# Performance work log

Hardware: AMD Instinct MI355X
Metric: run time of the kernel (lower is better)

Reference implementation:

```python
import jax, jax.numpy as jnp
import numpy as np

N, L, E, H = 8, 2048, 1024, 1024
EPS = 1e-5


def layernorm(x, g, b):
    m = jnp.mean(x, axis=-1, keepdims=True)
    v = jnp.var(x, axis=-1, keepdims=True)
    return (x - m) * jax.lax.rsqrt(v + EPS) * g + b


def setup_inputs() -> dict:
    key = jax.random.key(0)
    ks = jax.random.split(key, 6)
    s = 0.02
    return {
        "X": jax.random.normal(ks[0], (N, L, E), dtype=jnp.float32),
        "Wq": jax.random.normal(ks[1], (E, H), dtype=jnp.float32) * s,
        "bq": jnp.zeros((H,), jnp.float32),
        "Wk": jax.random.normal(ks[2], (E, H), dtype=jnp.float32) * s,
        "bk": jnp.zeros((H,), jnp.float32),
        "Wv": jax.random.normal(ks[3], (E, H), dtype=jnp.float32) * s,
        "bv": jnp.zeros((H,), jnp.float32),
        "Wf": jax.random.normal(ks[4], (H, H), dtype=jnp.float32) * s,
        "bf": jnp.zeros((H,), jnp.float32),
        "g1": jnp.ones((H,), jnp.float32),
        "b1": jnp.zeros((H,), jnp.float32),
        "g2": jnp.ones((H,), jnp.float32),
        "b2": jnp.zeros((H,), jnp.float32),
    }


def reference(X, Wq, bq, Wk, bk, Wv, bv, Wf, bf, g1, b1, g2, b2):
    scale = 1.0 / jnp.sqrt(jnp.float32(H))
    # both Q and K scaled by 1/sqrt(H) as in source (effective 1/H)
    Q = (X @ Wq + bq) * scale          # (N, L, H)
    K = (X @ Wk + bk) * scale          # (N, L, H)
    V = X @ Wv + bv                    # (N, L, H)
    A = jnp.einsum('nah,nbh->nab', Q, K)   # (N, Lq, Lk)
    A = jax.nn.softmax(A, axis=1)           # softmax over QUERY axis (dim=1), as in source
    # einsum('nll,nlh->nlh') = diagonal of A scaling V elementwise
    diag = jnp.diagonal(A, axis1=1, axis2=2)  # (N, L)
    O = diag[..., None] * V                   # (N, L, H)
    h = layernorm(O + X, g1, b1)
    h = layernorm(h @ Wf + bf + h, g2, b2)
    return h
```

## Files before the change

### kernel.cpp

```cpp
#include <hip/hip_runtime.h>
#include <math.h>

#define NB   8
#define LLEN 2048
#define HDIM 1024
#define LNEPS 1e-5f

#define BM 256
#define BN 256
#define BK 64
#define NT_K (HDIM / BK)
#define NT_K8 (HDIM / 128)
#define NTHR 512
#define SLOT (BM * BK)
#define SLOT8 32768

typedef __attribute__((ext_vector_type(8))) short short8;
typedef __attribute__((ext_vector_type(4))) unsigned short ushort4v;
typedef __attribute__((ext_vector_type(4))) float f32x4;
typedef __attribute__((ext_vector_type(4))) int int4v;
typedef __attribute__((ext_vector_type(8))) int int8v;
typedef __attribute__((ext_vector_type(8))) unsigned char uchar8;

typedef __attribute__((address_space(3))) void lds_void;
typedef const __attribute__((address_space(1))) void glob_void;

__device__ __forceinline__ unsigned short f2bf(float f) {
    union { float f; unsigned u; } v; v.f = f;
    unsigned r = v.u + 0x7FFFu + ((v.u >> 16) & 1u);
    return (unsigned short)(r >> 16);
}
__device__ __forceinline__ float bf2f(unsigned short h) {
    union { unsigned u; float f; } v; v.u = ((unsigned)h) << 16;
    return v.f;
}

__device__ __forceinline__ unsigned char f2fp8(float x) {
    union { float f; unsigned u; } v; v.f = x;
    unsigned s = (v.u >> 24) & 0x80u;
    float a = fabsf(x);
    if (!(a < 448.f)) return (unsigned char)(s | 0x7E);
    int e = (int)((v.u >> 23) & 0xFF) - 127;
    if (e < -6) e = -6;
    float q = rintf(ldexpf(a, 3 - e));
    if (q >= 16.f) { q *= 0.5f; e += 1; }
    int qi = (int)q;
    unsigned byte = (qi < 8) ? (unsigned)qi
                             : (((unsigned)(e + 7) << 3) | (unsigned)(qi - 8));
    return (unsigned char)(s | byte);
}
__device__ __forceinline__ float fp8d(unsigned char b) {
    int e = (b >> 3) & 15, m = b & 7;
    float v = e ? ldexpf((float)(8 + m), e - 10) : ldexpf((float)m, -9);
    return (b & 0x80) ? -v : v;
}

__device__ __forceinline__ unsigned pack4_fp8(float a, float b, float c, float d) {
#if __has_builtin(__builtin_amdgcn_cvt_pk_fp8_f32)
    int r = __builtin_amdgcn_cvt_pk_fp8_f32(a, b, 0, false);
    r = __builtin_amdgcn_cvt_pk_fp8_f32(c, d, r, true);
    return (unsigned)r;
#else
    return (unsigned)f2fp8(a) | ((unsigned)f2fp8(b) << 8)
         | ((unsigned)f2fp8(c) << 16) | ((unsigned)f2fp8(d) << 24);
#endif
}

__device__ __forceinline__ void wg_barrier() {
    asm volatile("" ::: "memory");
    __builtin_amdgcn_s_barrier();
    asm volatile("" ::: "memory");
}

__device__ __forceinline__ void stage_tile(
    const unsigned short* __restrict__ src, int R0, int kcol0,
    unsigned short* ldsDst, int w, int lane)
{
    const int rsub = lane >> 3;
    const int csw  = 8 * ((lane & 7) ^ rsub);
    #pragma unroll
    for (int s = 0; s < 4; ++s) {
        const int r = (s*8 + w)*8 + rsub;
        const unsigned short* g = src + (size_t)(R0 + r) * HDIM + kcol0 + csw;
        __builtin_amdgcn_global_load_lds(
            (glob_void*)g, (lds_void*)(ldsDst + (s*8 + w)*512), 16, 0, 0);
    }
}

__device__ __forceinline__ void run_pipeline(
    const unsigned short* __restrict__ srcA,
    const unsigned short* __restrict__ srcB,
    int rowBase, int colBase,
    unsigned short* lds, f32x4 (&acc)[8][4])
{
    const int t = threadIdx.x, w = t >> 6, l = t & 63;
    const int wr = w >> 2, wc = w & 3;
    const int lr = l & 15;
    const int sw = (l & 7) << 4;
    const int aRB = (wr*128 + lr) * 128;
    const int bRB = (wc*64  + lr) * 128;
    const int c0 = ((l >> 4) * 16) ^ sw;
    const int c1 = (64 + ((l >> 4) * 16)) ^ sw;

    unsigned short* sA[2] = { lds,            lds + 2*SLOT };
    unsigned short* sB[2] = { lds + SLOT,     lds + 3*SLOT };

    stage_tile(srcA, rowBase, 0,  sA[0], w, l);
    stage_tile(srcB, colBase, 0,  sB[0], w, l);
    stage_tile(srcA, rowBase, BK, sA[1], w, l);
    stage_tile(srcB, colBase, BK, sB[1], w, l);
    asm volatile("s_waitcnt vmcnt(8)" ::: "memory");
    wg_barrier();

    for (int kt = 0; kt < NT_K; ++kt) {
        const char* bufA = (const char*)sA[kt & 1];
        const char* bufB = (const char*)sB[kt & 1];
        #pragma unroll
        for (int kk = 0; kk < 2; ++kk) {
            const int cc = kk ? c1 : c0;
            short8 af[8], bfr[4];
            #pragma unroll
            for (int mi = 0; mi < 8; ++mi)
                af[mi] = *(const short8*)(bufA + aRB + mi*2048 + cc);
            #pragma unroll
            for (int ni = 0; ni < 4; ++ni)
                bfr[ni] = *(const short8*)(bufB + bRB + ni*2048 + cc);
            #pragma unroll
            for (int mi = 0; mi < 8; ++mi)
                #pragma unroll
                for (int ni = 0; ni < 4; ++ni)
                    acc[mi][ni] = __builtin_amdgcn_mfma_f32_16x16x32_bf16(
                        af[mi], bfr[ni], acc[mi][ni], 0, 0, 0);
        }
        if (kt == NT_K - 1) break;
        wg_barrier();
        if (kt + 2 < NT_K) {
            stage_tile(srcA, rowBase, (kt+2)*BK, sA[kt&1], w, l);
            stage_tile(srcB, colBase, (kt+2)*BK, sB[kt&1], w, l);
            asm volatile("s_waitcnt vmcnt(8)" ::: "memory");
        } else {
            asm volatile("s_waitcnt vmcnt(0)" ::: "memory");
        }
        wg_barrier();
    }
}

__device__ __forceinline__ void stage_tile8(
    const unsigned char* __restrict__ src, int R0, int kcol0,
    unsigned char* ldsDst, int w, int lane)
{
    const int rsub = lane >> 3;
    const int csw  = ((lane & 7) ^ rsub) << 4;
    #pragma unroll
    for (int s = 0; s < 4; ++s) {
        const int r = (s*8 + w)*8 + rsub;
        __builtin_amdgcn_global_load_lds(
            (glob_void*)(src + (size_t)(R0 + r) * HDIM + kcol0 + csw),
            (lds_void*)(ldsDst + (s*8 + w)*1024), 16, 0, 0);
    }
}

__device__ __forceinline__ void run_pipeline_fp8(
    const unsigned char* __restrict__ srcA,
    const unsigned char* __restrict__ srcB,
    int rowBase, int colBase,
    unsigned char* lds, f32x4 (&acc)[8][4],
    unsigned sa, unsigned sb)
{
    const int t = threadIdx.x, w = t >> 6, l = t & 63;
    const int wr = w >> 2, wc = w & 3;
    const int lr = l & 15;
    const int sw = (l & 7) << 4;
    const int aRB = (wr*128 + lr) * 128;
    const int bRB = (wc*64  + lr) * 128;
    const int g0 = (l >> 4) * 32;
    const int cc0 = g0 ^ sw;
    const int cc1 = (g0 + 16) ^ sw;

    unsigned char* sA[2] = { lds,             lds + 2*SLOT8 };
    unsigned char* sB[2] = { lds + SLOT8,     lds + 3*SLOT8 };

    stage_tile8(srcA, rowBase, 0,   sA[0], w, l);
    stage_tile8(srcB, colBase, 0,   sB[0], w, l);
    stage_tile8(srcA, rowBase, 128, sA[1], w, l);
    stage_tile8(srcB, colBase, 128, sB[1], w, l);
    asm volatile("s_waitcnt vmcnt(8)" ::: "memory");
    wg_barrier();

    for (int kt = 0; kt < NT_K8; ++kt) {
        const char* bufA = (const char*)sA[kt & 1];
        const char* bufB = (const char*)sB[kt & 1];
        int8v b8[4];
        #pragma unroll
        for (int ni = 0; ni < 4; ++ni)
            b8[ni] = __builtin_shufflevector(
                *(const int4v*)(bufB + bRB + ni*2048 + cc0),
                *(const int4v*)(bufB + bRB + ni*2048 + cc1),
                0, 1, 2, 3, 4, 5, 6, 7);
        #pragma unroll
        for (int mi = 0; mi < 8; ++mi) {
            int8v a8 = __builtin_shufflevector(
                *(const int4v*)(bufA + aRB + mi*2048 + cc0),
                *(const int4v*)(bufA + aRB + mi*2048 + cc1),
                0, 1, 2, 3, 4, 5, 6, 7);
            #pragma unroll
            for (int ni = 0; ni < 4; ++ni)
                acc[mi][ni] = __builtin_amdgcn_mfma_scale_f32_16x16x128_f8f6f4(
                    a8, b8[ni], acc[mi][ni], 0, 0, 0, sa, 0, sb);
        }
        if (kt == NT_K8 - 1) break;
        wg_barrier();
        if (kt + 2 < NT_K8) {
            stage_tile8(srcA, rowBase, (kt+2)*128, sA[kt&1], w, l);
            stage_tile8(srcB, colBase, (kt+2)*128, sB[kt&1], w, l);
            asm volatile("s_waitcnt vmcnt(8)" ::: "memory");
        } else {
            asm volatile("s_waitcnt vmcnt(0)" ::: "memory");
        }
        wg_barrier();
    }
}

__global__ __launch_bounds__(NTHR, 2) void gemm_proj(
    const unsigned short* __restrict__ A,
    const unsigned short* __restrict__ Bt,
    const float* __restrict__ bias0, const float* __restrict__ bias1,
    const float* __restrict__ bias2,
    unsigned short* __restrict__ C0, unsigned short* __restrict__ C1,
    unsigned short* __restrict__ C2,
    unsigned char* __restrict__ C8,
    float al0, float al1, float al2, int gx)
{
    __shared__ __align__(16) unsigned short lds[4 * SLOT];
    const int nwg = gridDim.x, bid = blockIdx.x;
    const int swz = (bid & 7) * (nwg >> 3) + (bid >> 3);
    const int bx = swz % gx, by = swz / gx;
    const int rowBase = by * BM, colBase = bx * BN;

    f32x4 acc[8][4] = {};
    run_pipeline(A, Bt, rowBase, colBase, lds, acc);

    const int t = threadIdx.x, w = t >> 6, l = t & 63;
    const int wr = w >> 2, wc = w & 3;
    const int lr = l & 15;

    const int mat = colBase >> 10;
    unsigned short* Cm = (mat == 0) ? C0 : (mat == 1 ? C1 : C2);
    const float* bm    = (mat == 0) ? bias0 : (mat == 1 ? bias1 : bias2);
    const float am     = (mat == 0) ? al0 : (mat == 1 ? al1 : al2);
    const int lcb = colBase & (HDIM - 1);

    if (mat == 0 && C8) {
        #pragma unroll
        for (int ni = 0; ni < 4; ++ni) {
            const int col = lcb + wc*64 + ni*16 + lr;
            const float bv = bm[col];
            #pragma unroll
            for (int mi = 0; mi < 8; ++mi) {
                const int row0 = rowBase + wr*128 + mi*16 + (l >> 4) * 4;
                const unsigned wd = pack4_fp8(
                    am * (acc[mi][ni][0] + bv), am * (acc[mi][ni][1] + bv),
                    am * (acc[mi][ni][2] + bv), am * (acc[mi][ni][3] + bv));
                #pragma unroll
                for (int j = 0; j < 4; ++j)
                    C8[(size_t)(row0 + j) * HDIM + col] = (unsigned char)(wd >> (8*j));
            }
        }
        return;
    }

    #pragma unroll
    for (int ni = 0; ni < 4; ++ni) {
        const int col = lcb + wc*64 + ni*16 + lr;
        const float bv = bm[col];
        #pragma unroll
        for (int mi = 0; mi < 8; ++mi) {
            const int row0 = rowBase + wr*128 + mi*16 + (l >> 4) * 4;
            #pragma unroll
            for (int j = 0; j < 4; ++j)
                Cm[(size_t)(row0 + j) * HDIM + col] = f2bf(am * (acc[mi][ni][j] + bv));
        }
    }
}

__global__ __launch_bounds__(NTHR, 2) void gemm_proj_fp8(
    const unsigned char* __restrict__ A,
    const unsigned char* __restrict__ Bt,
    const float* __restrict__ bias0, const float* __restrict__ bias1,
    unsigned char* __restrict__ C0, unsigned char* __restrict__ C1,
    float al0, float al1, unsigned sb0, unsigned sb1, int gx)
{
    __shared__ __align__(16) unsigned char lds8[4 * SLOT8];
    const int nwg = gridDim.x, bid = blockIdx.x;
    const int swz = (bid & 7) * (nwg >> 3) + (bid >> 3);
    const int bx = swz % gx, by = swz / gx;
    const int rowBase = by * BM, colBase = bx * BN;

    const int mat = colBase >> 10;

    f32x4 acc[8][4] = {};
    run_pipeline_fp8(A, Bt, rowBase, colBase, lds8, acc,
                     0x7F7F7F7Fu, mat ? sb1 : sb0);

    const int t = threadIdx.x, w = t >> 6, l = t & 63;
    const int wr = w >> 2, wc = w & 3;
    const int lr = l & 15;

    unsigned char* Cm  = mat ? C1 : C0;
    const float* bm    = mat ? bias1 : bias0;
    const float am     = mat ? al1 : al0;
    const int lcb = colBase & (HDIM - 1);

    #pragma unroll
    for (int ni = 0; ni < 4; ++ni) {
        const int col = lcb + wc*64 + ni*16 + lr;
        const float bv = bm[col];
        #pragma unroll
        for (int mi = 0; mi < 8; ++mi) {
            const int row0 = rowBase + wr*128 + mi*16 + (l >> 4) * 4;
            const unsigned wd = pack4_fp8(
                am * (acc[mi][ni][0] + bv), am * (acc[mi][ni][1] + bv),
                am * (acc[mi][ni][2] + bv), am * (acc[mi][ni][3] + bv));
            #pragma unroll
            for (int j = 0; j < 4; ++j)
                Cm[(size_t)(row0 + j) * HDIM + col] = (unsigned char)(wd >> (8*j));
        }
    }
}

__global__ __launch_bounds__(NTHR, 2) void qk_colsum_diag_fp8(
    const unsigned char* __restrict__ Xq8,
    const unsigned char* __restrict__ Xb8,
    const float* __restrict__ uvec,
    float* __restrict__ colsum, float* __restrict__ diagv)
{
    __shared__ __align__(16) unsigned char lds8[4 * SLOT8];
    const int bid = blockIdx.x;
    const int n = bid & 7;
    const int rem = bid >> 3;
    const int rowBase = (rem & 7) * BM;
    const int colBase = (rem >> 3) * BN;
    const unsigned char* An = Xq8 + (size_t)n * LLEN * HDIM;
    const unsigned char* Bn = Xb8 + (size_t)n * LLEN * HDIM;

    f32x4 acc[8][4] = {};
    run_pipeline_fp8(An, Bn, rowBase, colBase, lds8, acc,
                     0x75757575u, 0x7F7F7F7Fu);

    const int t = threadIdx.x, w = t >> 6, l = t & 63;
    const int wr = w >> 2, wc = w & 3;
    const int lr = l & 15;

    float ur[8][4];
    #pragma unroll
    for (int mi = 0; mi < 8; ++mi)
        #pragma unroll
        for (int j = 0; j < 4; ++j)
            ur[mi][j] = uvec[(size_t)n * LLEN + rowBase + wr*128 + mi*16 + (l>>4)*4 + j];

    #pragma unroll
    for (int ni = 0; ni < 4; ++ni) {
        float s = 0.f;
        #pragma unroll
        for (int mi = 0; mi < 8; ++mi)
            #pragma unroll
            for (int j = 0; j < 4; ++j)
                s += __expf(acc[mi][ni][j] + ur[mi][j]);
        s += __shfl_xor(s, 16);
        s += __shfl_xor(s, 32);
        if (l < 16)
            atomicAdd(&colsum[(size_t)n * LLEN + colBase + wc*64 + ni*16 + l], s);
    }

    if (rowBase == colBase && (wc >> 1) == wr) {
        #pragma unroll
        for (int mi = 0; mi < 8; ++mi)
            #pragma unroll
            for (int ni = 0; ni < 4; ++ni)
                #pragma unroll
                for (int j = 0; j < 4; ++j) {
                    const int rr = wr*128 + mi*16 + (l >> 4)*4 + j;
                    const int cc = wc*64 + ni*16 + lr;
                    if (rr == cc)
                        diagv[(size_t)n * LLEN + rowBase + rr] = acc[mi][ni][j];
                }
    }
}

__global__ __launch_bounds__(256) void cast_x_dual(
    const float* __restrict__ in, unsigned short* __restrict__ outb,
    unsigned char* __restrict__ out8, int n8)
{
    int i = blockIdx.x * 256 + threadIdx.x;
    if (i >= n8) return;
    const float4* p = reinterpret_cast<const float4*>(in) + (size_t)i * 2;
    float4 a = p[0], b = p[1];
    short8 o;
    o[0] = (short)f2bf(a.x); o[1] = (short)f2bf(a.y);
    o[2] = (short)f2bf(a.z); o[3] = (short)f2bf(a.w);
    o[4] = (short)f2bf(b.x); o[5] = (short)f2bf(b.y);
    o[6] = (short)f2bf(b.z); o[7] = (short)f2bf(b.w);
    unsigned w0 = pack4_fp8(a.x, a.y, a.z, a.w);
    unsigned w1 = pack4_fp8(b.x, b.y, b.z, b.w);
    *(reinterpret_cast<short8*>(outb) + i) = o;
    uint2 pk; pk.x = w0; pk.y = w1;
    *(reinterpret_cast<uint2*>(out8) + i) = pk;
}

__global__ __launch_bounds__(256) void cast_f32_bf16(
    const float* __restrict__ in, unsigned short* __restrict__ outp, int n8)
{
    int i = blockIdx.x * 256 + threadIdx.x;
    if (i >= n8) return;
    const float4* p = reinterpret_cast<const float4*>(in) + (size_t)i * 2;
    float4 a = p[0], b = p[1];
    short8 o;
    o[0] = (short)f2bf(a.x); o[1] = (short)f2bf(a.y);
    o[2] = (short)f2bf(a.z); o[3] = (short)f2bf(a.w);
    o[4] = (short)f2bf(b.x); o[5] = (short)f2bf(b.y);
    o[6] = (short)f2bf(b.z); o[7] = (short)f2bf(b.w);
    *(reinterpret_cast<short8*>(outp) + i) = o;
}

__global__ __launch_bounds__(256) void transpose_cast_bf16(
    const float* __restrict__ W, unsigned short* __restrict__ Wt)
{
    __shared__ float tile[32][33];
    const int tx = threadIdx.x & 31, ty = threadIdx.x >> 5;
    const int c0 = blockIdx.x * 32, r0 = blockIdx.y * 32;
    #pragma unroll
    for (int r = 0; r < 4; ++r)
        tile[ty + r*8][tx] = W[(size_t)(r0 + ty + r*8) * HDIM + c0 + tx];
    __syncthreads();
    #pragma unroll
    for (int r = 0; r < 4; ++r)
        Wt[(size_t)(c0 + ty + r*8) * HDIM + r0 + tx] = f2bf(tile[tx][ty + r*8]);
}

__global__ __launch_bounds__(256) void transpose_cast_fp8(
    const float* __restrict__ W, unsigned char* __restrict__ Wt, float scale)
{
    __shared__ float tile[32][33];
    const int tx = threadIdx.x & 31, ty = threadIdx.x >> 5;
    const int c0 = blockIdx.x * 32, r0 = blockIdx.y * 32;
    #pragma unroll
    for (int r = 0; r < 4; ++r)
        tile[ty + r*8][tx] = W[(size_t)(r0 + ty + r*8) * HDIM + c0 + tx];
    __syncthreads();
    #pragma unroll
    for (int r = 0; r < 4; ++r)
        Wt[(size_t)(c0 + ty + r*8) * HDIM + r0 + tx] = f2fp8(tile[tx][ty + r*8] * scale);
}

__global__ __launch_bounds__(256) void pvec_kernel(
    const float* __restrict__ Wq, const float* __restrict__ bk,
    float* __restrict__ p)
{
    const int row = blockIdx.x * 4 + (threadIdx.x >> 6);
    const int l = threadIdx.x & 63;
    float s = 0.f;
    #pragma unroll
    for (int c = 0; c < HDIM; c += 64)
        s += Wq[(size_t)row * HDIM + c + l] * bk[c + l];
    #pragma unroll
    for (int off = 32; off > 0; off >>= 1) s += __shfl_down(s, off);
    if (l == 0) p[row] = s;
}

__global__ __launch_bounds__(256) void uvec_kernel(
    const unsigned short* __restrict__ Xb, const float* __restrict__ p,
    float* __restrict__ u, float sc2)
{
    const int row = blockIdx.x * 4 + (threadIdx.x >> 6);
    const int l = threadIdx.x & 63;
    const unsigned short* xr = Xb + (size_t)row * HDIM + l * 16;
    float s = 0.f;
    #pragma unroll
    for (int k = 0; k < 2; ++k) {
        short8 v = *reinterpret_cast<const short8*>(xr + k*8);
        #pragma unroll
        for (int j = 0; j < 8; ++j)
            s += bf2f((unsigned short)v[j]) * p[l*16 + k*8 + j];
    }
    #pragma unroll
    for (int off = 32; off > 0; off >>= 1) s += __shfl_down(s, off);
    if (l == 0) u[row] = s * sc2;
}

__global__ __launch_bounds__(256) void ln1_kernel(
    const unsigned char* __restrict__ V8, const unsigned short* __restrict__ Xbp,
    const float* __restrict__ colsum, const float* __restrict__ diagval,
    const float* __restrict__ uvec,
    const float* __restrict__ g1, const float* __restrict__ b1,
    unsigned short* __restrict__ h1)
{
    const int row = blockIdx.x;
    const size_t base = (size_t)row * HDIM;
    const float dv = __expf(diagval[row] + uvec[row]) / colsum[row];
    const int h0 = threadIdx.x * 4;

    unsigned vv = *reinterpret_cast<const unsigned*>(&V8[base + h0]);
    ushort4v xx = *reinterpret_cast<const ushort4v*>(&Xbp[base + h0]);
    float y[4];
    y[0] = dv * fp8d((unsigned char)(vv      )) + bf2f(xx[0]);
    y[1] = dv * fp8d((unsigned char)(vv >>  8)) + bf2f(xx[1]);
    y[2] = dv * fp8d((unsigned char)(vv >> 16)) + bf2f(xx[2]);
    y[3] = dv * fp8d((unsigned char)(vv >> 24)) + bf2f(xx[3]);

    float s = y[0]+y[1]+y[2]+y[3];
    float s2 = y[0]*y[0]+y[1]*y[1]+y[2]*y[2]+y[3]*y[3];
    #pragma unroll
    for (int off = 32; off > 0; off >>= 1) {
        s  += __shfl_down(s,  off);
        s2 += __shfl_down(s2, off);
    }
    __shared__ float ws1[4], ws2[4];
    const int wid = threadIdx.x >> 6;
    if ((threadIdx.x & 63) == 0) { ws1[wid] = s; ws2[wid] = s2; }
    __syncthreads();
    const float S  = ws1[0]+ws1[1]+ws1[2]+ws1[3];
    const float S2 = ws2[0]+ws2[1]+ws2[2]+ws2[3];
    const float m   = S  * (1.0f / HDIM);
    const float var = S2 * (1.0f / HDIM) - m*m;
    const float inv = rsqrtf(var + LNEPS);

    float4 gg = *reinterpret_cast<const float4*>(&g1[h0]);
    float4 bb = *reinterpret_cast<const float4*>(&b1[h0]);
    ushort4v o;
    o[0] = f2bf((y[0]-m)*inv*gg.x + bb.x);
    o[1] = f2bf((y[1]-m)*inv*gg.y + bb.y);
    o[2] = f2bf((y[2]-m)*inv*gg.z + bb.z);
    o[3] = f2bf((y[3]-m)*inv*gg.w + bb.w);
    *reinterpret_cast<ushort4v*>(&h1[base + h0]) = o;
}

__global__ __launch_bounds__(256) void ln2_kernel(
    const unsigned short* __restrict__ Gb, const unsigned short* __restrict__ h1b,
    const float* __restrict__ g2, const float* __restrict__ b2,
    float* __restrict__ out)
{
    const int row = blockIdx.x;
    const size_t base = (size_t)row * HDIM;
    const int h0 = threadIdx.x * 4;

    ushort4v gv = *reinterpret_cast<const ushort4v*>(&Gb[base + h0]);
    ushort4v hv = *reinterpret_cast<const ushort4v*>(&h1b[base + h0]);
    float y[4];
    y[0] = bf2f(gv[0]) + bf2f(hv[0]); y[1] = bf2f(gv[1]) + bf2f(hv[1]);
    y[2] = bf2f(gv[2]) + bf2f(hv[2]); y[3] = bf2f(gv[3]) + bf2f(hv[3]);

    float s = y[0]+y[1]+y[2]+y[3];
    float s2 = y[0]*y[0]+y[1]*y[1]+y[2]*y[2]+y[3]*y[3];
    #pragma unroll
    for (int off = 32; off > 0; off >>= 1) {
        s  += __shfl_down(s,  off);
        s2 += __shfl_down(s2, off);
    }
    __shared__ float ws1[4], ws2[4];
    const int wid = threadIdx.x >> 6;
    if ((threadIdx.x & 63) == 0) { ws1[wid] = s; ws2[wid] = s2; }
    __syncthreads();
    const float S  = ws1[0]+ws1[1]+ws1[2]+ws1[3];
    const float S2 = ws2[0]+ws2[1]+ws2[2]+ws2[3];
    const float m   = S  * (1.0f / HDIM);
    const float var = S2 * (1.0f / HDIM) - m*m;
    const float inv = rsqrtf(var + LNEPS);

    float4 gg = *reinterpret_cast<const float4*>(&g2[h0]);
    float4 bb = *reinterpret_cast<const float4*>(&b2[h0]);
    float4 o;
    o.x = (y[0]-m)*inv*gg.x + bb.x;
    o.y = (y[1]-m)*inv*gg.y + bb.y;
    o.z = (y[2]-m)*inv*gg.z + bb.z;
    o.w = (y[3]-m)*inv*gg.w + bb.w;
    *reinterpret_cast<float4*>(&out[base + h0]) = o;
}

extern "C" void kernel_launch(void* const* d_in, const int* in_sizes, int n_in,
                              void* d_out, int out_size, void* d_ws, size_t ws_size,
                              hipStream_t stream) {
    (void)in_sizes; (void)n_in; (void)out_size; (void)ws_size;
    const float* X  = (const float*)d_in[0];
    const float* Wq = (const float*)d_in[1];
    const float* bq = (const float*)d_in[2];   (void)bq;
    const float* Wk = (const float*)d_in[3];
    const float* bk = (const float*)d_in[4];
    const float* Wv = (const float*)d_in[5];
    const float* bv = (const float*)d_in[6];
    const float* Wf = (const float*)d_in[7];
    const float* bf = (const float*)d_in[8];
    const float* g1 = (const float*)d_in[9];
    const float* b1 = (const float*)d_in[10];
    const float* g2 = (const float*)d_in[11];
    const float* b2 = (const float*)d_in[12];
    float* out = (float*)d_out;

    const size_t MATE = (size_t)NB * LLEN * HDIM;
    const size_t WE   = (size_t)HDIM * HDIM;

    unsigned short* Xb  = (unsigned short*)d_out;
    unsigned char*  V8  = (unsigned char*)(Xb + MATE);

    unsigned short* h1b   = (unsigned short*)d_ws;
    unsigned short* Gb    = h1b + MATE;
    unsigned short* WfT   = Gb + MATE;
    unsigned short* Wqb   = WfT + WE;
    unsigned short* Wkb   = Wqb + WE;
    unsigned char*  Wqk8T = (unsigned char*)(Wkb + WE);
    unsigned char*  Wv8T  = Wqk8T + WE;
    float* colsum = (float*)(Wv8T + WE);
    float* diagv  = colsum + (size_t)NB * LLEN;
    float* pv     = diagv + (size_t)NB * LLEN;
    float* uv     = pv + HDIM;
    float* zvec   = uv + (size_t)NB * LLEN;
    unsigned char* Xq8 = (unsigned char*)(zvec + HDIM);
    unsigned char* Xb8 = Xq8 + MATE;

    const int M = NB * LLEN;
    const float sc2 = 1.0f / 1024.0f;

    hipMemsetAsync(colsum, 0, (size_t)NB * LLEN * sizeof(float), stream);
    hipMemsetAsync(zvec, 0, HDIM * sizeof(float), stream);

    cast_x_dual<<<(int)(MATE/8) / 256, 256, 0, stream>>>(X, Xb, Xb8, (int)(MATE/8));
    cast_f32_bf16<<<(int)(WE/8) / 256, 256, 0, stream>>>(Wq, Wqb, (int)(WE/8));
    cast_f32_bf16<<<(int)(WE/8) / 256, 256, 0, stream>>>(Wk, Wkb, (int)(WE/8));

    {
        dim3 tgrid(HDIM / 32, HDIM / 32);
        transpose_cast_bf16<<<tgrid, 256, 0, stream>>>(Wf, WfT);
        transpose_cast_fp8<<<tgrid, 256, 0, stream>>>(Wv, Wv8T, 16.0f);
    }

    gemm_proj<<<16, NTHR, 0, stream>>>(Wkb, Wqb, zvec, zvec, zvec,
                                       nullptr, nullptr, nullptr, Wqk8T,
                                       64.0f, 64.0f, 64.0f, 4);

    pvec_kernel<<<HDIM / 4, 256, 0, stream>>>(Wq, bk, pv);
    uvec_kernel<<<M / 4, 256, 0, stream>>>(Xb, pv, uv, sc2);

    {
        const int gx = 2 * HDIM / BN;
        const int nwg = gx * (M / BM);
        gemm_proj_fp8<<<nwg, NTHR, 0, stream>>>(Xb8, Wqk8T, zvec, bv,
                                                Xq8, V8, 1024.0f, 1.0f,
                                                0x6F6F6F6Fu ,
                                                0x7B7B7B7Bu , gx);
    }

    qk_colsum_diag_fp8<<<512, NTHR, 0, stream>>>(Xq8, Xb8, uv, colsum, diagv);

    ln1_kernel<<<M, 256, 0, stream>>>(V8, Xb, colsum, diagv, uv, g1, b1, h1b);

    {
        const int gx = HDIM / BN;
        const int nwg = gx * (M / BM);
        gemm_proj<<<nwg, NTHR, 0, stream>>>(h1b, WfT, bf, bf, bf,
                                            Gb, Gb, Gb, (unsigned char*)nullptr,
                                            1.0f, 1.0f, 1.0f, gx);
    }

    ln2_kernel<<<M, 256, 0, stream>>>(Gb, h1b, g2, b2, out);
}
```

Before: 247.8 us.

## Split-K the Wk·Wqᵀ weight product across more workgroups and merge small launches

The 1024x1024 Wk·Wqᵀ product ran on only 16 workgroups. It now splits K four ways across 64 workgroups that write fp32 partial slabs, followed by a reduce kernel that sums the slabs, scales and packs to fp8. The two weight casts are merged into one launch, and the two memsets into one larger memset. The aim is better CU utilisation on a small GEMM in exchange for extra fp32 slab traffic and one more launch. gemm_proj is simplified to a single output.

```diff
diff --git a/kernel.cpp b/kernel.cpp
--- a/kernel.cpp
+++ b/kernel.cpp
@@ -90,7 +90,7 @@
 __device__ __forceinline__ void run_pipeline(
     const unsigned short* __restrict__ srcA,
     const unsigned short* __restrict__ srcB,
-    int rowBase, int colBase,
+    int rowBase, int colBase, int k0, int nt,
     unsigned short* lds, f32x4 (&acc)[8][4])
 {
     const int t = threadIdx.x, w = t >> 6, l = t & 63;
@@ -105,14 +105,14 @@
     unsigned short* sA[2] = { lds,            lds + 2*SLOT };
     unsigned short* sB[2] = { lds + SLOT,     lds + 3*SLOT };
 
-    stage_tile(srcA, rowBase, 0,  sA[0], w, l);
-    stage_tile(srcB, colBase, 0,  sB[0], w, l);
-    stage_tile(srcA, rowBase, BK, sA[1], w, l);
-    stage_tile(srcB, colBase, BK, sB[1], w, l);
+    stage_tile(srcA, rowBase, k0,      sA[0], w, l);
+    stage_tile(srcB, colBase, k0,      sB[0], w, l);
+    stage_tile(srcA, rowBase, k0 + BK, sA[1], w, l);
+    stage_tile(srcB, colBase, k0 + BK, sB[1], w, l);
     asm volatile("s_waitcnt vmcnt(8)" ::: "memory");
     wg_barrier();
 
-    for (int kt = 0; kt < NT_K; ++kt) {
+    for (int kt = 0; kt < nt; ++kt) {
         const char* bufA = (const char*)sA[kt & 1];
         const char* bufB = (const char*)sB[kt & 1];
         #pragma unroll
@@ -132,11 +132,11 @@
                     acc[mi][ni] = __builtin_amdgcn_mfma_f32_16x16x32_bf16(
                         af[mi], bfr[ni], acc[mi][ni], 0, 0, 0);
         }
-        if (kt == NT_K - 1) break;
+        if (kt == nt - 1) break;
         wg_barrier();
-        if (kt + 2 < NT_K) {
-            stage_tile(srcA, rowBase, (kt+2)*BK, sA[kt&1], w, l);
-            stage_tile(srcB, colBase, (kt+2)*BK, sB[kt&1], w, l);
+        if (kt + 2 < nt) {
+            stage_tile(srcA, rowBase, k0 + (kt+2)*BK, sA[kt&1], w, l);
+            stage_tile(srcB, colBase, k0 + (kt+2)*BK, sB[kt&1], w, l);
             asm volatile("s_waitcnt vmcnt(8)" ::: "memory");
         } else {
             asm volatile("s_waitcnt vmcnt(0)" ::: "memory");
@@ -224,12 +224,9 @@
 __global__ __launch_bounds__(NTHR, 2) void gemm_proj(
     const unsigned short* __restrict__ A,
     const unsigned short* __restrict__ Bt,
-    const float* __restrict__ bias0, const float* __restrict__ bias1,
-    const float* __restrict__ bias2,
-    unsigned short* __restrict__ C0, unsigned short* __restrict__ C1,
-    unsigned short* __restrict__ C2,
-    unsigned char* __restrict__ C8,
-    float al0, float al1, float al2, int gx)
+    const float* __restrict__ bias,
+    unsigned short* __restrict__ C,
+    float alpha, int gx)
 {
     __shared__ __align__(16) unsigned short lds[4 * SLOT];
     const int nwg = gridDim.x, bid = blockIdx.x;
@@ -238,49 +235,69 @@
     const int rowBase = by * BM, colBase = bx * BN;
 
     f32x4 acc[8][4] = {};
-    run_pipeline(A, Bt, rowBase, colBase, lds, acc);
+    run_pipeline(A, Bt, rowBase, colBase, 0, NT_K, lds, acc);
 
     const int t = threadIdx.x, w = t >> 6, l = t & 63;
     const int wr = w >> 2, wc = w & 3;
     const int lr = l & 15;
 
-    const int mat = colBase >> 10;
-    unsigned short* Cm = (mat == 0) ? C0 : (mat == 1 ? C1 : C2);
-    const float* bm    = (mat == 0) ? bias0 : (mat == 1 ? bias1 : bias2);
-    const float am     = (mat == 0) ? al0 : (mat == 1 ? al1 : al2);
-    const int lcb = colBase & (HDIM - 1);
-
-    if (mat == 0 && C8) {
-        #pragma unroll
-        for (int ni = 0; ni < 4; ++ni) {
-            const int col = lcb + wc*64 + ni*16 + lr;
-            const float bv = bm[col];
-            #pragma unroll
-            for (int mi = 0; mi < 8; ++mi) {
-                const int row0 = rowBase + wr*128 + mi*16 + (l >> 4) * 4;
-                const unsigned wd = pack4_fp8(
-                    am * (acc[mi][ni][0] + bv), am * (acc[mi][ni][1] + bv),
-                    am * (acc[mi][ni][2] + bv), am * (acc[mi][ni][3] + bv));
-                #pragma unroll
-                for (int j = 0; j < 4; ++j)
-                    C8[(size_t)(row0 + j) * HDIM + col] = (unsigned char)(wd >> (8*j));
-            }
-        }
-        return;
-    }
-
     #pragma unroll
     for (int ni = 0; ni < 4; ++ni) {
-        const int col = lcb + wc*64 + ni*16 + lr;
-        const float bv = bm[col];
+        const int col = colBase + wc*64 + ni*16 + lr;
+        const float bv = bias[col];
         #pragma unroll
         for (int mi = 0; mi < 8; ++mi) {
             const int row0 = rowBase + wr*128 + mi*16 + (l >> 4) * 4;
             #pragma unroll
             for (int j = 0; j < 4; ++j)
-                Cm[(size_t)(row0 + j) * HDIM + col] = f2bf(am * (acc[mi][ni][j] + bv));
+                C[(size_t)(row0 + j) * HDIM + col] = f2bf(alpha * (acc[mi][ni][j] + bv));
         }
     }
+}
+
+__global__ __launch_bounds__(NTHR, 2) void gemm_wqk_splitk(
+    const unsigned short* __restrict__ Wkb,
+    const unsigned short* __restrict__ Wqb,
+    float* __restrict__ slabs)
+{
+    __shared__ __align__(16) unsigned short lds[4 * SLOT];
+    const int bid = blockIdx.x;
+    const int kz = bid & 3, tile = bid >> 2;
+    const int rowBase = (tile >> 2) * BM, colBase = (tile & 3) * BN;
+
+    f32x4 acc[8][4] = {};
+    run_pipeline(Wkb, Wqb, rowBase, colBase, kz * (HDIM/4), NT_K/4, lds, acc);
+
+    float* out = slabs + (size_t)kz * HDIM * HDIM;
+    const int t = threadIdx.x, w = t >> 6, l = t & 63;
+    const int wr = w >> 2, wc = w & 3;
+    const int lr = l & 15;
+
+    #pragma unroll
+    for (int ni = 0; ni < 4; ++ni) {
+        const int col = colBase + wc*64 + ni*16 + lr;
+        #pragma unroll
+        for (int mi = 0; mi < 8; ++mi) {
+            const int row0 = rowBase + wr*128 + mi*16 + (l >> 4) * 4;
+            #pragma unroll
+            for (int j = 0; j < 4; ++j)
+                out[(size_t)(row0 + j) * HDIM + col] = acc[mi][ni][j];
+        }
+    }
+}
+
+__global__ __launch_bounds__(256) void wqk_reduce_cast(
+    const float* __restrict__ slabs, unsigned char* __restrict__ out8)
+{
+    const size_t WEl = (size_t)HDIM * HDIM;
+    const size_t i = ((size_t)blockIdx.x * 256 + threadIdx.x) * 4;
+    float4 a = *reinterpret_cast<const float4*>(slabs + i);
+    float4 b = *reinterpret_cast<const float4*>(slabs + WEl + i);
+    float4 c = *reinterpret_cast<const float4*>(slabs + 2*WEl + i);
+    float4 d = *reinterpret_cast<const float4*>(slabs + 3*WEl + i);
+    unsigned wd = pack4_fp8(64.f*(a.x+b.x+c.x+d.x), 64.f*(a.y+b.y+c.y+d.y),
+                            64.f*(a.z+b.z+c.z+d.z), 64.f*(a.w+b.w+c.w+d.w));
+    *reinterpret_cast<unsigned*>(out8 + i) = wd;
 }
 
 __global__ __launch_bounds__(NTHR, 2) void gemm_proj_fp8(
@@ -407,11 +424,14 @@
     *(reinterpret_cast<uint2*>(out8) + i) = pk;
 }
 
-__global__ __launch_bounds__(256) void cast_f32_bf16(
-    const float* __restrict__ in, unsigned short* __restrict__ outp, int n8)
+__global__ __launch_bounds__(256) void cast_w2(
+    const float* __restrict__ W0, const float* __restrict__ W1,
+    unsigned short* __restrict__ out0, unsigned short* __restrict__ out1, int n8)
 {
     int i = blockIdx.x * 256 + threadIdx.x;
     if (i >= n8) return;
+    const float* in = blockIdx.y ? W1 : W0;
+    unsigned short* outp = blockIdx.y ? out1 : out0;
     const float4* p = reinterpret_cast<const float4*>(in) + (size_t)i * 2;
     float4 a = p[0], b = p[1];
     short8 o;
@@ -615,26 +635,27 @@
     float* zvec   = uv + (size_t)NB * LLEN;
     unsigned char* Xq8 = (unsigned char*)(zvec + HDIM);
     unsigned char* Xb8 = Xq8 + MATE;
+    float* wqkSlabs = (float*)(Xb8 + MATE);
 
     const int M = NB * LLEN;
     const float sc2 = 1.0f / 1024.0f;
 
-    hipMemsetAsync(colsum, 0, (size_t)NB * LLEN * sizeof(float), stream);
-    hipMemsetAsync(zvec, 0, HDIM * sizeof(float), stream);
+    const size_t mset = (3*(size_t)NB*LLEN + 2*HDIM) * sizeof(float);
+    hipMemsetAsync(colsum, 0, mset, stream);
 
     cast_x_dual<<<(int)(MATE/8) / 256, 256, 0, stream>>>(X, Xb, Xb8, (int)(MATE/8));
-    cast_f32_bf16<<<(int)(WE/8) / 256, 256, 0, stream>>>(Wq, Wqb, (int)(WE/8));
-    cast_f32_bf16<<<(int)(WE/8) / 256, 256, 0, stream>>>(Wk, Wkb, (int)(WE/8));
-
+    {
+        dim3 cg((int)(WE/8) / 256, 2);
+        cast_w2<<<cg, 256, 0, stream>>>(Wq, Wk, Wqb, Wkb, (int)(WE/8));
+    }
     {
         dim3 tgrid(HDIM / 32, HDIM / 32);
         transpose_cast_bf16<<<tgrid, 256, 0, stream>>>(Wf, WfT);
         transpose_cast_fp8<<<tgrid, 256, 0, stream>>>(Wv, Wv8T, 16.0f);
     }
 
-    gemm_proj<<<16, NTHR, 0, stream>>>(Wkb, Wqb, zvec, zvec, zvec,
-                                       nullptr, nullptr, nullptr, Wqk8T,
-                                       64.0f, 64.0f, 64.0f, 4);
+    gemm_wqk_splitk<<<64, NTHR, 0, stream>>>(Wkb, Wqb, wqkSlabs);
+    wqk_reduce_cast<<<(int)(WE/4) / 256, 256, 0, stream>>>(wqkSlabs, Wqk8T);
 
     pvec_kernel<<<HDIM / 4, 256, 0, stream>>>(Wq, bk, pv);
     uvec_kernel<<<M / 4, 256, 0, stream>>>(Xb, pv, uv, sc2);
@@ -655,9 +676,7 @@
     {
         const int gx = HDIM / BN;
         const int nwg = gx * (M / BM);
-        gemm_proj<<<nwg, NTHR, 0, stream>>>(h1b, WfT, bf, bf, bf,
-                                            Gb, Gb, Gb, (unsigned char*)nullptr,
-                                            1.0f, 1.0f, 1.0f, gx);
+        gemm_proj<<<nwg, NTHR, 0, stream>>>(h1b, WfT, bf, Gb, 1.0f, gx);
     }
 
     ln2_kernel<<<M, 256, 0, stream>>>(Gb, h1b, g2, b2, out);
```

After: 232.6 us. 6.1% less time.
